# Kernel optimization log

Measured on AMD Instinct MI355X. Metric: run time of the kernel, lower is better.

Reference implementation:

```python
import jax, jax.numpy as jnp
import numpy as np

EPS = 1e-5

def _inorm(t, axes):
    m = t.mean(axis=axes, keepdims=True)
    v = t.var(axis=axes, keepdims=True)
    return (t - m) * jax.lax.rsqrt(v + EPS)

def setup_inputs() -> dict:
    key = jax.random.key(0)
    ks = jax.random.split(key, 7)
    b, c, d, o, h, w = 2, 128, 128, 128, 16, 16
    maxlen = 256
    return {
        "x": jax.random.normal(ks[0], (b, c, h, w), jnp.float32),
        "y": jax.random.normal(ks[1], (b, d, h, w), jnp.float32),
        "pos_emb": jax.random.normal(ks[2], (maxlen, c), jnp.float32) * 0.02,
        "w1": jax.random.normal(ks[3], (o, 2 * c + d), jnp.float32) * 0.05,
        "b1": jax.random.normal(ks[4], (o,), jnp.float32) * 0.01,
        "w2": jax.random.normal(ks[5], (o, o), jnp.float32) * 0.05,
        "b2": jax.random.normal(ks[6], (o,), jnp.float32) * 0.01,
    }

def reference(x, y, pos_emb, w1, b1, w2, b2):
    b, c, h, w = x.shape
    d = y.shape[1]
    hw = h * w
    # positional embedding: tokens = arange(hw), permute to channel-first
    pos = pos_emb[:hw].T.reshape(c, h, w)  # [c,h,w]
    x = x + pos[None]
    x = jax.nn.relu(_inorm(x, (2, 3)))
    y = jax.nn.relu(_inorm(y, (2, 3)))
    xf = x.reshape(b, c, hw)
    yf = y.reshape(b, d, hw)
    # conv1x1 over cat([x_i, x_j, y]) splits into three GEMMs (same math):
    Wi, Wj, Wy = w1[:, :c], w1[:, c:2 * c], w1[:, 2 * c:]
    A = jnp.einsum('oc,bcj->boj', Wi, xf)                    # varies along j
    B = jnp.einsum('oc,bci->boi', Wj, xf) + jnp.einsum('od,bdi->boi', Wy, yf)  # varies along i
    z = A[:, :, None, :] + B[:, :, :, None] + b1[None, :, None, None]  # [b,o,hw,hw]
    z = jax.nn.relu(_inorm(z, (2, 3)))
    # second conv1x1 then sum over dim=3 commutes: w2 @ sum_j z + hw*b2
    s = z.sum(axis=3)  # [b,o,hw]
    out = jnp.einsum('po,boi->bpi', w2, s) + hw * b2[None, :, None]
    return out.reshape(b, -1, h, w)
```

## Files before the change

kernel.cpp:

```cpp
#include <hip/hip_runtime.h>

#define HW 256
#define C  128

__global__ __launch_bounds__(1024) void k_rel(
        const float* __restrict__ x, const float* __restrict__ y,
        const float* __restrict__ pos, const float* __restrict__ w1,
        float* __restrict__ s_out) {
    __shared__ float pA[16][256];
    __shared__ float pB[16][256];
    __shared__ float red[16][4];
    __shared__ float aj[256];
    __shared__ float bi[256];
    __shared__ float wrow[384];

    const int t    = threadIdx.x;
    const int l    = t & 255;
    const int g    = t >> 8;
    const int w    = t >> 6;
    const int lane = t & 63;
    const int bo   = blockIdx.x;
    const int b    = bo >> 7;
    const int o    = bo & 127;

    if (t < 384) wrow[t] = w1[o * 384 + t];
    __syncthreads();

    const float* xb = x + b * (C * HW);
    const float* yb = y + b * (C * HW);
    const int j4 = lane * 4;

    float A4[4]  = {0.f, 0.f, 0.f, 0.f};
    float B4[4]  = {0.f, 0.f, 0.f, 0.f};

    #pragma unroll
    for (int r = 0; r < 8; ++r) {
        const int c = w * 8 + r;
        const float4 xv = *reinterpret_cast<const float4*>(xb + c * HW + j4);
        float v[4] = { xv.x + pos[(j4 + 0) * C + c],
                       xv.y + pos[(j4 + 1) * C + c],
                       xv.z + pos[(j4 + 2) * C + c],
                       xv.w + pos[(j4 + 3) * C + c] };
        float s1 = v[0] + v[1] + v[2] + v[3];
        float s2 = v[0]*v[0] + v[1]*v[1] + v[2]*v[2] + v[3]*v[3];
        #pragma unroll
        for (int off = 32; off > 0; off >>= 1) {
            s1 += __shfl_xor(s1, off, 64);
            s2 += __shfl_xor(s2, off, 64);
        }
        const float m    = s1 * (1.0f / 256.0f);
        const float var  = s2 * (1.0f / 256.0f) - m * m;
        const float istd = rsqrtf(var + 1e-5f);
        const float wi = wrow[c], wj = wrow[128 + c];
        #pragma unroll
        for (int k = 0; k < 4; ++k) {
            float nv = (v[k] - m) * istd;
            nv = nv > 0.f ? nv : 0.f;
            A4[k] = fmaf(wi, nv, A4[k]);
            B4[k] = fmaf(wj, nv, B4[k]);
        }
    }
    #pragma unroll
    for (int r = 0; r < 8; ++r) {
        const int d = w * 8 + r;
        const float4 yv = *reinterpret_cast<const float4*>(yb + d * HW + j4);
        float v[4] = { yv.x, yv.y, yv.z, yv.w };
        float s1 = v[0] + v[1] + v[2] + v[3];
        float s2 = v[0]*v[0] + v[1]*v[1] + v[2]*v[2] + v[3]*v[3];
        #pragma unroll
        for (int off = 32; off > 0; off >>= 1) {
            s1 += __shfl_xor(s1, off, 64);
            s2 += __shfl_xor(s2, off, 64);
        }
        const float m    = s1 * (1.0f / 256.0f);
        const float var  = s2 * (1.0f / 256.0f) - m * m;
        const float istd = rsqrtf(var + 1e-5f);
        const float wy = wrow[256 + d];
        #pragma unroll
        for (int k = 0; k < 4; ++k) {
            float nv = (v[k] - m) * istd;
            nv = nv > 0.f ? nv : 0.f;
            B4[k] = fmaf(wy, nv, B4[k]);
        }
    }

    #pragma unroll
    for (int k = 0; k < 4; ++k) {
        pA[w][j4 + k] = A4[k];
        pB[w][j4 + k] = B4[k];
    }
    __syncthreads();

    float Af = 0.f, Bf = 0.f;
    if (t < 256) {
        #pragma unroll
        for (int ww = 0; ww < 16; ++ww) { Af += pA[ww][l]; Bf += pB[ww][l]; }
    }

    float rA = Af, rA2 = Af * Af, rB = Bf, rB2 = Bf * Bf;
    #pragma unroll
    for (int off = 32; off > 0; off >>= 1) {
        rA  += __shfl_xor(rA,  off, 64);
        rA2 += __shfl_xor(rA2, off, 64);
        rB  += __shfl_xor(rB,  off, 64);
        rB2 += __shfl_xor(rB2, off, 64);
    }
    if (lane == 0) { red[w][0] = rA; red[w][1] = rA2; red[w][2] = rB; red[w][3] = rB2; }
    __syncthreads();
    float sA = 0.f, sA2 = 0.f, sB = 0.f, sB2 = 0.f;
    #pragma unroll
    for (int ww = 0; ww < 16; ++ww) {
        sA += red[ww][0]; sA2 += red[ww][1]; sB += red[ww][2]; sB2 += red[ww][3];
    }
    const float mA   = sA  * (1.0f / 256.0f);
    const float mB   = sB  * (1.0f / 256.0f);
    const float varA = sA2 * (1.0f / 256.0f) - mA * mA;
    const float varB = sB2 * (1.0f / 256.0f) - mB * mB;
    const float istd = rsqrtf(varA + varB + 1e-5f);

    if (t < 256) {
        aj[l] = (Af - mA) * istd;
        bi[l] = (Bf - mB) * istd;
    }
    __syncthreads();

    const float bb = bi[l];
    float acc = 0.f;
    const int j0 = g * 64;
    #pragma unroll
    for (int jj = 0; jj < 64; ++jj) {
        const float zv = aj[j0 + jj] + bb;
        acc += (zv > 0.f ? zv : 0.f);
    }
    pA[g][l] = acc;
    __syncthreads();
    if (t < 256)
        s_out[bo * HW + l] = pA[0][l] + pA[1][l] + pA[2][l] + pA[3][l];
}

__global__ __launch_bounds__(1024) void k_out(
        const float* __restrict__ s_in, const float* __restrict__ w2,
        const float* __restrict__ b2, float* __restrict__ out) {
    __shared__ float wrow[128];
    __shared__ float pacc[4][256];
    const int t  = threadIdx.x;
    const int l  = t & 255;
    const int g  = t >> 8;
    const int bp = blockIdx.x;
    const int b  = bp >> 7;
    const int p  = bp & 127;
    if (t < 128) wrow[t] = w2[p * 128 + t];
    __syncthreads();
    const float* sb = s_in + b * (C * HW);
    float acc = 0.f;
    const int o0 = g * 32;
    #pragma unroll
    for (int oo = 0; oo < 32; ++oo)
        acc = fmaf(wrow[o0 + oo], sb[(o0 + oo) * HW + l], acc);
    pacc[g][l] = acc;
    __syncthreads();
    if (t < 256)
        out[bp * HW + l] = pacc[0][l] + pacc[1][l] + pacc[2][l] + pacc[3][l]
                           + 256.0f * b2[p];
}

extern "C" void kernel_launch(void* const* d_in, const int* in_sizes, int n_in,
                              void* d_out, int out_size, void* d_ws, size_t ws_size,
                              hipStream_t stream) {
    const float* x   = (const float*)d_in[0];
    const float* y   = (const float*)d_in[1];
    const float* pos = (const float*)d_in[2];
    const float* w1  = (const float*)d_in[3];
    const float* w2  = (const float*)d_in[5];
    const float* b2  = (const float*)d_in[6];
    float* out = (float*)d_out;

    float* s = (float*)d_ws;

    k_rel<<<256, 1024, 0, stream>>>(x, y, pos, w1, s);
    k_out<<<256, 1024, 0, stream>>>(s, w2, b2, out);
}
```

Baseline: 85.15 us.

## Hoist instance norm into separate kernel to avoid per-output-channel recomputation

Adds a k_norm kernel that normalizes x (with positional embedding) and y once and writes the results to workspace. Previously each of the 256 k_rel blocks recomputed the norm stats and the strided pos gathers for every channel. k_rel now does plain FMAs on the pre-normalized data, reading weights straight from global memory. The relu-sum loop is vectorized with float4 LDS reads, and k_out is restructured to use 16 waves with float4 loads. The cost is a third kernel launch and an extra workspace round trip.

```diff
diff --git a/kernel.cpp b/kernel.cpp
--- a/kernel.cpp
+++ b/kernel.cpp
@@ -3,87 +3,85 @@
 #define HW 256
 #define C  128
 
+__device__ __forceinline__ float relu(float v) { return v > 0.f ? v : 0.f; }
+
+__global__ __launch_bounds__(64) void k_norm(
+        const float* __restrict__ x, const float* __restrict__ y,
+        const float* __restrict__ pos, float* __restrict__ xn, float* __restrict__ yn) {
+    const int blk  = blockIdx.x;
+    const int lane = threadIdx.x;
+    const int j4   = lane * 4;
+
+    float v0, v1, v2, v3;
+    float* dst;
+    if (blk < 256) {
+        const int c = blk & 127;
+        const float4 xv = *reinterpret_cast<const float4*>(x + blk * HW + j4);
+        v0 = xv.x + pos[(j4 + 0) * C + c];
+        v1 = xv.y + pos[(j4 + 1) * C + c];
+        v2 = xv.z + pos[(j4 + 2) * C + c];
+        v3 = xv.w + pos[(j4 + 3) * C + c];
+        dst = xn + blk * HW;
+    } else {
+        const int bc = blk - 256;
+        const float4 yv = *reinterpret_cast<const float4*>(y + bc * HW + j4);
+        v0 = yv.x; v1 = yv.y; v2 = yv.z; v3 = yv.w;
+        dst = yn + bc * HW;
+    }
+    float s1 = v0 + v1 + v2 + v3;
+    float s2 = v0*v0 + v1*v1 + v2*v2 + v3*v3;
+    #pragma unroll
+    for (int off = 32; off > 0; off >>= 1) {
+        s1 += __shfl_xor(s1, off, 64);
+        s2 += __shfl_xor(s2, off, 64);
+    }
+    const float m    = s1 * (1.0f / 256.0f);
+    const float var  = s2 * (1.0f / 256.0f) - m * m;
+    const float istd = rsqrtf(var + 1e-5f);
+    float4 r;
+    r.x = relu((v0 - m) * istd);
+    r.y = relu((v1 - m) * istd);
+    r.z = relu((v2 - m) * istd);
+    r.w = relu((v3 - m) * istd);
+    *reinterpret_cast<float4*>(dst + j4) = r;
+}
+
 __global__ __launch_bounds__(1024) void k_rel(
-        const float* __restrict__ x, const float* __restrict__ y,
-        const float* __restrict__ pos, const float* __restrict__ w1,
-        float* __restrict__ s_out) {
+        const float* __restrict__ xn, const float* __restrict__ yn,
+        const float* __restrict__ w1, float* __restrict__ s_out) {
     __shared__ float pA[16][256];
     __shared__ float pB[16][256];
     __shared__ float red[16][4];
-    __shared__ float aj[256];
+    __shared__ __align__(16) float aj[256];
     __shared__ float bi[256];
-    __shared__ float wrow[384];
 
     const int t    = threadIdx.x;
     const int l    = t & 255;
     const int g    = t >> 8;
     const int w    = t >> 6;
     const int lane = t & 63;
+    const int j4   = lane * 4;
     const int bo   = blockIdx.x;
     const int b    = bo >> 7;
     const int o    = bo & 127;
 
-    if (t < 384) wrow[t] = w1[o * 384 + t];
-    __syncthreads();
+    const float* xb = xn + b * (C * HW);
+    const float* yb = yn + b * (C * HW);
+    const float* wr = w1 + o * 384;
 
-    const float* xb = x + b * (C * HW);
-    const float* yb = y + b * (C * HW);
-    const int j4 = lane * 4;
-
-    float A4[4]  = {0.f, 0.f, 0.f, 0.f};
-    float B4[4]  = {0.f, 0.f, 0.f, 0.f};
-
+    float A4[4] = {0.f, 0.f, 0.f, 0.f};
+    float B4[4] = {0.f, 0.f, 0.f, 0.f};
     #pragma unroll
     for (int r = 0; r < 8; ++r) {
         const int c = w * 8 + r;
+        const float wi = wr[c], wj = wr[128 + c], wy = wr[256 + c];
         const float4 xv = *reinterpret_cast<const float4*>(xb + c * HW + j4);
-        float v[4] = { xv.x + pos[(j4 + 0) * C + c],
-                       xv.y + pos[(j4 + 1) * C + c],
-                       xv.z + pos[(j4 + 2) * C + c],
-                       xv.w + pos[(j4 + 3) * C + c] };
-        float s1 = v[0] + v[1] + v[2] + v[3];
-        float s2 = v[0]*v[0] + v[1]*v[1] + v[2]*v[2] + v[3]*v[3];
-        #pragma unroll
-        for (int off = 32; off > 0; off >>= 1) {
-            s1 += __shfl_xor(s1, off, 64);
-            s2 += __shfl_xor(s2, off, 64);
-        }
-        const float m    = s1 * (1.0f / 256.0f);
-        const float var  = s2 * (1.0f / 256.0f) - m * m;
-        const float istd = rsqrtf(var + 1e-5f);
-        const float wi = wrow[c], wj = wrow[128 + c];
-        #pragma unroll
-        for (int k = 0; k < 4; ++k) {
-            float nv = (v[k] - m) * istd;
-            nv = nv > 0.f ? nv : 0.f;
-            A4[k] = fmaf(wi, nv, A4[k]);
-            B4[k] = fmaf(wj, nv, B4[k]);
-        }
+        const float4 yv = *reinterpret_cast<const float4*>(yb + c * HW + j4);
+        A4[0] = fmaf(wi, xv.x, A4[0]);  B4[0] = fmaf(wj, xv.x, fmaf(wy, yv.x, B4[0]));
+        A4[1] = fmaf(wi, xv.y, A4[1]);  B4[1] = fmaf(wj, xv.y, fmaf(wy, yv.y, B4[1]));
+        A4[2] = fmaf(wi, xv.z, A4[2]);  B4[2] = fmaf(wj, xv.z, fmaf(wy, yv.z, B4[2]));
+        A4[3] = fmaf(wi, xv.w, A4[3]);  B4[3] = fmaf(wj, xv.w, fmaf(wy, yv.w, B4[3]));
     }
-    #pragma unroll
-    for (int r = 0; r < 8; ++r) {
-        const int d = w * 8 + r;
-        const float4 yv = *reinterpret_cast<const float4*>(yb + d * HW + j4);
-        float v[4] = { yv.x, yv.y, yv.z, yv.w };
-        float s1 = v[0] + v[1] + v[2] + v[3];
-        float s2 = v[0]*v[0] + v[1]*v[1] + v[2]*v[2] + v[3]*v[3];
-        #pragma unroll
-        for (int off = 32; off > 0; off >>= 1) {
-            s1 += __shfl_xor(s1, off, 64);
-            s2 += __shfl_xor(s2, off, 64);
-        }
-        const float m    = s1 * (1.0f / 256.0f);
-        const float var  = s2 * (1.0f / 256.0f) - m * m;
-        const float istd = rsqrtf(var + 1e-5f);
-        const float wy = wrow[256 + d];
-        #pragma unroll
-        for (int k = 0; k < 4; ++k) {
-            float nv = (v[k] - m) * istd;
-            nv = nv > 0.f ? nv : 0.f;
-            B4[k] = fmaf(wy, nv, B4[k]);
-        }
-    }
-
     #pragma unroll
     for (int k = 0; k < 4; ++k) {
         pA[w][j4 + k] = A4[k];
@@ -125,12 +123,12 @@
     __syncthreads();
 
     const float bb = bi[l];
+    const float4* aj4 = reinterpret_cast<const float4*>(aj);
     float acc = 0.f;
-    const int j0 = g * 64;
     #pragma unroll
-    for (int jj = 0; jj < 64; ++jj) {
-        const float zv = aj[j0 + jj] + bb;
-        acc += (zv > 0.f ? zv : 0.f);
+    for (int jj = 0; jj < 16; ++jj) {
+        const float4 a = aj4[g * 16 + jj];
+        acc += relu(a.x + bb) + relu(a.y + bb) + relu(a.z + bb) + relu(a.w + bb);
     }
     pA[g][l] = acc;
     __syncthreads();
@@ -141,27 +139,40 @@
 __global__ __launch_bounds__(1024) void k_out(
         const float* __restrict__ s_in, const float* __restrict__ w2,
         const float* __restrict__ b2, float* __restrict__ out) {
-    __shared__ float wrow[128];
-    __shared__ float pacc[4][256];
-    const int t  = threadIdx.x;
-    const int l  = t & 255;
-    const int g  = t >> 8;
-    const int bp = blockIdx.x;
-    const int b  = bp >> 7;
-    const int p  = bp & 127;
-    if (t < 128) wrow[t] = w2[p * 128 + t];
+    __shared__ float pacc[16][256];
+    const int t    = threadIdx.x;
+    const int l    = t & 255;
+    const int w    = t >> 6;
+    const int lane = t & 63;
+    const int j4   = lane * 4;
+    const int bp   = blockIdx.x;
+    const int b    = bp >> 7;
+    const int p    = bp & 127;
+
+    const float* sb = s_in + b * (C * HW);
+    const float* wr = w2 + p * 128;
+    float a0 = 0.f, a1 = 0.f, a2 = 0.f, a3 = 0.f;
+    #pragma unroll
+    for (int r = 0; r < 8; ++r) {
+        const int o = w * 8 + r;
+        const float wv = wr[o];
+        const float4 sv = *reinterpret_cast<const float4*>(sb + o * HW + j4);
+        a0 = fmaf(wv, sv.x, a0);
+        a1 = fmaf(wv, sv.y, a1);
+        a2 = fmaf(wv, sv.z, a2);
+        a3 = fmaf(wv, sv.w, a3);
+    }
+    pacc[w][j4 + 0] = a0;
+    pacc[w][j4 + 1] = a1;
+    pacc[w][j4 + 2] = a2;
+    pacc[w][j4 + 3] = a3;
     __syncthreads();
-    const float* sb = s_in + b * (C * HW);
-    float acc = 0.f;
-    const int o0 = g * 32;
-    #pragma unroll
-    for (int oo = 0; oo < 32; ++oo)
-        acc = fmaf(wrow[o0 + oo], sb[(o0 + oo) * HW + l], acc);
-    pacc[g][l] = acc;
-    __syncthreads();
-    if (t < 256)
-        out[bp * HW + l] = pacc[0][l] + pacc[1][l] + pacc[2][l] + pacc[3][l]
-                           + 256.0f * b2[p];
+    if (t < 256) {
+        float acc = 256.0f * b2[p];
+        #pragma unroll
+        for (int ww = 0; ww < 16; ++ww) acc += pacc[ww][l];
+        out[bp * HW + l] = acc;
+    }
 }
 
 extern "C" void kernel_launch(void* const* d_in, const int* in_sizes, int n_in,
@@ -175,8 +186,11 @@
     const float* b2  = (const float*)d_in[6];
     float* out = (float*)d_out;
 
-    float* s = (float*)d_ws;
+    float* xn = (float*)d_ws;
+    float* yn = xn + 65536;
+    float* s  = yn + 65536;
 
-    k_rel<<<256, 1024, 0, stream>>>(x, y, pos, w1, s);
-    k_out<<<256, 1024, 0, stream>>>(s, w2, b2, out);
+    k_norm<<<512,  64, 0, stream>>>(x, y, pos, xn, yn);
+    k_rel <<<256, 1024, 0, stream>>>(xn, yn, w1, s);
+    k_out <<<256, 1024, 0, stream>>>(s, w2, b2, out);
 }
```

Result: faster. 77.18 us (-9.4%).
